# Optimization experiments

Hardware: AMD Instinct MI355X
Metric: run time of the kernel (lower is better)

Reference implementation:

```python
import jax, jax.numpy as jnp
import numpy as np

# Fuzzy system constants (from _init_fuzzy_system)
X1_C = jnp.arange(5.0)                 # x1 gauss centers 0,1,2,3,4 ; sigma 1
X2_C = jnp.arange(5.0) * 45.0          # x2 gauss centers 0,45,90,135,180 ; sigma 45
OUT_C = jnp.array([-0.3, 0.1, 0.5, 0.9, 1.3], dtype=jnp.float32)  # consequent centers ; sigma 0.3
Z = jnp.asarray(np.arange(-0.3, 1.31, 0.01), dtype=jnp.float32)   # 161-pt output universe

# Mamdani rules: list per consequent level of (x1_level, x2_level) OR-terms, levels XS..XL = 0..4
RULES = [
    [(2, 4), (3, 4), (3, 3), (4, 3), (4, 4)],            # -> coupling XS
    [(1, 4), (2, 3), (3, 2), (4, 1)],                    # -> S
    [(0, 4), (1, 3), (2, 2), (3, 1), (4, 0)],            # -> M
    [(0, 3), (1, 2), (2, 1), (3, 0)],                    # -> L
    [(0, 2), (0, 1), (0, 0), (1, 1), (1, 0), (2, 0)],    # -> XL
]


def gauss(x, c, s):
    return jnp.exp(-0.5 * ((x - c) / s) ** 2)


def setup_inputs() -> dict:
    key = jax.random.key(0)
    k1, k2, k3, k4 = jax.random.split(key, 4)
    N, E, D = 50000, 1000000, 8
    h = jax.random.normal(k1, (N, D), dtype=jnp.float32)
    src_idx = jax.random.randint(k2, (E,), 0, N, dtype=jnp.int32)
    dst_idx = jax.random.randint(k3, (E,), 0, N, dtype=jnp.int32)
    etypes = jax.random.randint(k4, (E,), 0, 3, dtype=jnp.int32)
    return {"h": h, "src_idx": src_idx, "dst_idx": dst_idx, "etypes": etypes}


def reference(h, src_idx, dst_idx, etypes):
    # edge vector: dst['h'] - src['h']
    v = h[dst_idx] - h[src_idx]                       # [E, D]
    # Ante_generator: x1 = |v| (distance, clipped to universe), x2 = angle(v, e1) in degrees
    n = jnp.sqrt(jnp.sum(v * v, axis=-1) + 1e-12)     # [E]
    x1 = jnp.clip(n, 0.0, 4.0)
    cosang = jnp.clip(v[:, 0] / n, -0.999999, 0.999999)
    x2 = jnp.degrees(jnp.arccos(cosang))              # [E] in [0, 180]
    # antecedent memberships
    mu1 = gauss(x1[:, None], X1_C[None, :], 1.0)      # [E, 5]
    mu2 = gauss(x2[:, None], X2_C[None, :], 45.0)     # [E, 5]
    zmf = gauss(Z[None, :], OUT_C[:, None], 0.3)      # [5, 161]
    # Mamdani: rule activation = max over OR-terms of min(mu1, mu2);
    # implication = min(act, consequent mf); aggregation = max over rules
    agg = jnp.zeros((x1.shape[0], Z.shape[0]), dtype=h.dtype)  # [E, 161]
    for r, pairs in enumerate(RULES):
        act = jnp.max(
            jnp.stack([jnp.minimum(mu1[:, i], mu2[:, j]) for i, j in pairs], axis=-1),
            axis=-1,
        )                                             # [E]
        agg = jnp.maximum(agg, jnp.minimum(act[:, None], zmf[r][None, :]))
    # centroid defuzzification
    coupling_degree = jnp.sum(agg * Z[None, :], axis=-1) / jnp.sum(agg, axis=-1)
    return coupling_degree
```

## Files before the change

### kernel.cpp

```cpp
#include <hip/hip_runtime.h>
#include <hip/hip_fp16.h>

typedef int   vi4 __attribute__((ext_vector_type(4)));
typedef float vf4 __attribute__((ext_vector_type(4)));

static constexpr double cexp_taylor(double x) {
    double s = 1.0, t = 1.0;
    for (int i = 1; i < 40; ++i) { t = t * x / (double)i; s += t; }
    return s;
}
static constexpr double cpow_int(double b, long e) {
    double r = 1.0, p = b;
    while (e > 0) { if (e & 1) r *= p; p *= p; e >>= 1; }
    return r;
}
struct ZmfTab { float v[5][161]; };
static constexpr ZmfTab make_zmf() {
    ZmfTab t{};
    const double c0 = cexp_taylor(-1.0 / 1800.0);
    for (int r = 0; r < 5; ++r)
        for (int k = 0; k < 161; ++k) {
            long d = (long)(k - 40 * r);
            t.v[r][k] = (float)cpow_int(c0, d * d);
        }
    return t;
}
static constexpr ZmfTab ZMF = make_zmf();
static constexpr float ZCUT = 1e-4f;

__device__ __forceinline__ float fuzzy_F(float x1, float u)
{
    float m1[5], m2[5];
#pragma unroll
    for (int i = 0; i < 5; ++i) {
        float d1 = x1 - (float)i;
        float d2 = u  - (float)i;
        m1[i] = __expf(-0.5f * d1 * d1);
        m2[i] = __expf(-0.5f * d2 * d2);
    }

    float a0 = fmaxf(fmaxf(fminf(m1[2], m2[4]), fminf(m1[3], m2[4])),
               fmaxf(fminf(m1[3], m2[3]),
               fmaxf(fminf(m1[4], m2[3]), fminf(m1[4], m2[4]))));
    float a1 = fmaxf(fmaxf(fminf(m1[1], m2[4]), fminf(m1[2], m2[3])),
               fmaxf(fminf(m1[3], m2[2]), fminf(m1[4], m2[1])));
    float a2 = fmaxf(fmaxf(fminf(m1[0], m2[4]), fminf(m1[1], m2[3])),
               fmaxf(fminf(m1[2], m2[2]),
               fmaxf(fminf(m1[3], m2[1]), fminf(m1[4], m2[0]))));
    float a3 = fmaxf(fmaxf(fminf(m1[0], m2[3]), fminf(m1[1], m2[2])),
               fmaxf(fminf(m1[2], m2[1]), fminf(m1[3], m2[0])));
    float a4 = fmaxf(fmaxf(fmaxf(fminf(m1[0], m2[2]), fminf(m1[0], m2[1])),
               fmaxf(fminf(m1[0], m2[0]), fminf(m1[1], m2[1]))),
               fmaxf(fminf(m1[1], m2[0]), fminf(m1[2], m2[0])));
    float a[5] = {a0, a1, a2, a3, a4};

    float s0 = 0.0f, s1 = 0.0f;
#pragma unroll
    for (int k = 0; k < 161; ++k) {
        float m = -1.0f;
        bool first = true;
#pragma unroll
        for (int r = 0; r < 5; ++r) {
            if (ZMF.v[r][k] >= ZCUT) {
                float tmin = fminf(a[r], ZMF.v[r][k]);
                m = first ? tmin : fmaxf(m, tmin);
                first = false;
            }
        }
        s0 += m;
        s1 = fmaf(m, (float)k, s1);
    }
    return fmaf(0.01f, s1 / s0, -0.3f);
}

#define PN 70
#define VN 71
#define TAB_U4 ((PN * PN) / 2)

struct H8 { __half2 p0, p1, p2, p3; };

__global__ __launch_bounds__(256) void build_pack_kernel(
    const float4* __restrict__ h4, __half* __restrict__ gtab,
    __half2* __restrict__ hp, int N, int nA)
{
    int b = blockIdx.x;
    if (b < nA) {
        int idx = b * 256 + threadIdx.x;
        if (idx >= VN * VN) return;
        int i = idx / VN;
        int j = idx - i * VN;
        const float hstep = 4.0f / (float)PN;
        __half f = __float2half_rn(fuzzy_F((float)i * hstep, (float)j * hstep));
        if (i < PN && j < PN) gtab[4 * (i * PN + j) + 0]           = f;
        if (i < PN && j > 0)  gtab[4 * (i * PN + j - 1) + 1]       = f;
        if (i > 0 && j < PN)  gtab[4 * ((i - 1) * PN + j) + 2]     = f;
        if (i > 0 && j > 0)   gtab[4 * ((i - 1) * PN + j - 1) + 3] = f;
    } else {
        int r = (b - nA) * 256 + threadIdx.x;
        if (r >= N) return;
        float4 a = h4[2 * r], c = h4[2 * r + 1];
        __half2* o = hp + 4 * r;
        o[0] = __floats2half2_rn(a.x, a.y);
        o[1] = __floats2half2_rn(a.z, a.w);
        o[2] = __floats2half2_rn(c.x, c.y);
        o[3] = __floats2half2_rn(c.z, c.w);
    }
}

__device__ __forceinline__ float edge_eval(
    const H8* __restrict__ hp, const uint2* __restrict__ stab,
    int si, int di)
{
    H8 s = hp[si];
    H8 d = hp[di];

    float2 d0 = __half22float2(__hsub2(d.p0, s.p0));
    float2 d1 = __half22float2(__hsub2(d.p1, s.p1));
    float2 d2 = __half22float2(__hsub2(d.p2, s.p2));
    float2 d3 = __half22float2(__hsub2(d.p3, s.p3));

    float ss = fmaf(d0.x, d0.x, fmaf(d0.y, d0.y, fmaf(d1.x, d1.x, fmaf(d1.y, d1.y,
               fmaf(d2.x, d2.x, fmaf(d2.y, d2.y, fmaf(d3.x, d3.x,
               fmaf(d3.y, d3.y, 1e-12f))))))));

    float rn = rsqrtf(ss);
    float n  = ss * rn;
    float x1 = fminf(n, 4.0f);

    float c = d0.x * rn;
    c = fminf(fmaxf(c, -0.999999f), 0.999999f);

    float ac = fabsf(c);
    float t  = sqrtf(1.0f - ac);
    float p  = fmaf(fmaf(fmaf(-0.0187293f, ac, 0.0742610f), ac, -0.2121144f),
                    ac, 1.5707288f);
    float r0 = t * p;
    float acosv = (c < 0.0f) ? (3.14159265358979f - r0) : r0;
    float u = acosv * 1.27323954473516f;

    const float sc = (float)PN * 0.25f;
    float t1 = x1 * sc;
    float t2 = u  * sc;
    int i1 = min((int)t1, PN - 1);
    int i2 = min((int)t2, PN - 1);
    float f1 = t1 - (float)i1;
    float f2 = t2 - (float)i2;

    uint2 pk = stab[i1 * PN + i2];
    float2 lo2 = __half22float2(__builtin_bit_cast(__half2, pk.x));
    float2 hi2 = __half22float2(__builtin_bit_cast(__half2, pk.y));
    float lo = fmaf(f2, lo2.y - lo2.x, lo2.x);
    float hi = fmaf(f2, hi2.y - hi2.x, hi2.x);
    return fmaf(f1, hi - lo, lo);
}

__global__ __launch_bounds__(512, 8) void fuzzy_coupling_kernel(
    const H8*    __restrict__ hp,
    const int*   __restrict__ src,
    const int*   __restrict__ dst,
    const uint4* __restrict__ gtab4,
    float*       __restrict__ out,
    int E)
{
    __shared__ uint4 stab4[TAB_U4];
    for (int k = threadIdx.x; k < TAB_U4; k += 512) stab4[k] = gtab4[k];
    __syncthreads();
    const uint2* stab = (const uint2*)stab4;

    int t = blockIdx.x * 512 + threadIdx.x;
    int e0 = 4 * t;
    if (e0 >= E) return;

    if (e0 + 3 < E) {
        vi4 sp = __builtin_nontemporal_load((const vi4*)src + t);
        vi4 dp = __builtin_nontemporal_load((const vi4*)dst + t);
        float r0 = edge_eval(hp, stab, sp.x, dp.x);
        float r1 = edge_eval(hp, stab, sp.y, dp.y);
        float r2 = edge_eval(hp, stab, sp.z, dp.z);
        float r3 = edge_eval(hp, stab, sp.w, dp.w);
        vf4 res; res.x = r0; res.y = r1; res.z = r2; res.w = r3;
        __builtin_nontemporal_store(res, (vf4*)out + t);
    } else {
        for (int e = e0; e < E; ++e)
            out[e] = edge_eval(hp, stab, src[e], dst[e]);
    }
}

extern "C" void kernel_launch(void* const* d_in, const int* in_sizes, int n_in,
                              void* d_out, int out_size, void* d_ws, size_t ws_size,
                              hipStream_t stream)
{
    const float* h   = (const float*)d_in[0];
    const int*   src = (const int*)d_in[1];
    const int*   dst = (const int*)d_in[2];
    float* out = (float*)d_out;

    __half*  gtab = (__half*)d_ws;
    __half2* hp   = (__half2*)((char*)d_ws + 65536);

    int N = in_sizes[0] / 8;
    int E = in_sizes[1];

    int nA = (VN * VN + 255) / 256;
    int nB = (N + 255) / 256;
    build_pack_kernel<<<nA + nB, 256, 0, stream>>>(
        (const float4*)h, gtab, hp, N, nA);

    int threads = (E + 3) / 4;
    int grid = (threads + 511) / 512;
    fuzzy_coupling_kernel<<<grid, 512, 0, stream>>>(
        (const H8*)hp, src, dst, (const uint4*)gtab, out, E);
}
```

Measured before the change: 79.03 us.

## Store fuzzy lookup table as plain fp32 grid and process two edges per thread

Replaces the packed fp16 quad-corner lookup table with a plain fp32 (VN x VN) grid. Each lookup now does four LDS reads instead of one 8-byte read, and the table holds only the grid values, so the build kernel writes each value once. It also halves the edges per thread from four to two, doubling the thread and block count. That gives more parallelism for the random gathers, but each block now repeats the shared-table load for fewer edges, and the LDS reads per edge go up.

```diff
diff --git a/kernel.cpp b/kernel.cpp
--- a/kernel.cpp
+++ b/kernel.cpp
@@ -1,8 +1,8 @@
 #include <hip/hip_runtime.h>
 #include <hip/hip_fp16.h>
 
-typedef int   vi4 __attribute__((ext_vector_type(4)));
-typedef float vf4 __attribute__((ext_vector_type(4)));
+typedef int   vi2 __attribute__((ext_vector_type(2)));
+typedef float vf2 __attribute__((ext_vector_type(2)));
 
 static constexpr double cexp_taylor(double x) {
     double s = 1.0, t = 1.0;
@@ -75,12 +75,13 @@
 
 #define PN 70
 #define VN 71
-#define TAB_U4 ((PN * PN) / 2)
+#define TAB_F  ((VN * VN + 3) & ~3)
+#define TAB_U4 (TAB_F / 4)
 
 struct H8 { __half2 p0, p1, p2, p3; };
 
 __global__ __launch_bounds__(256) void build_pack_kernel(
-    const float4* __restrict__ h4, __half* __restrict__ gtab,
+    const float4* __restrict__ h4, float* __restrict__ gtab,
     __half2* __restrict__ hp, int N, int nA)
 {
     int b = blockIdx.x;
@@ -90,11 +91,7 @@
         int i = idx / VN;
         int j = idx - i * VN;
         const float hstep = 4.0f / (float)PN;
-        __half f = __float2half_rn(fuzzy_F((float)i * hstep, (float)j * hstep));
-        if (i < PN && j < PN) gtab[4 * (i * PN + j) + 0]           = f;
-        if (i < PN && j > 0)  gtab[4 * (i * PN + j - 1) + 1]       = f;
-        if (i > 0 && j < PN)  gtab[4 * ((i - 1) * PN + j) + 2]     = f;
-        if (i > 0 && j > 0)   gtab[4 * ((i - 1) * PN + j - 1) + 3] = f;
+        gtab[idx] = fuzzy_F((float)i * hstep, (float)j * hstep);
     } else {
         int r = (b - nA) * 256 + threadIdx.x;
         if (r >= N) return;
@@ -108,7 +105,7 @@
 }
 
 __device__ __forceinline__ float edge_eval(
-    const H8* __restrict__ hp, const uint2* __restrict__ stab,
+    const H8* __restrict__ hp, const float* __restrict__ stab,
     int si, int di)
 {
     H8 s = hp[si];
@@ -146,11 +143,13 @@
     float f1 = t1 - (float)i1;
     float f2 = t2 - (float)i2;
 
-    uint2 pk = stab[i1 * PN + i2];
-    float2 lo2 = __half22float2(__builtin_bit_cast(__half2, pk.x));
-    float2 hi2 = __half22float2(__builtin_bit_cast(__half2, pk.y));
-    float lo = fmaf(f2, lo2.y - lo2.x, lo2.x);
-    float hi = fmaf(f2, hi2.y - hi2.x, hi2.x);
+    const float* ptab = stab + (i1 * VN + i2);
+    float v00 = ptab[0];
+    float v01 = ptab[1];
+    float v10 = ptab[VN];
+    float v11 = ptab[VN + 1];
+    float lo = fmaf(f2, v01 - v00, v00);
+    float hi = fmaf(f2, v11 - v10, v10);
     return fmaf(f1, hi - lo, lo);
 }
 
@@ -162,27 +161,24 @@
     float*       __restrict__ out,
     int E)
 {
-    __shared__ uint4 stab4[TAB_U4];
-    for (int k = threadIdx.x; k < TAB_U4; k += 512) stab4[k] = gtab4[k];
+    __shared__ float stab[TAB_F];
+    uint4* s4 = (uint4*)stab;
+    for (int k = threadIdx.x; k < TAB_U4; k += 512) s4[k] = gtab4[k];
     __syncthreads();
-    const uint2* stab = (const uint2*)stab4;
 
     int t = blockIdx.x * 512 + threadIdx.x;
-    int e0 = 4 * t;
+    int e0 = 2 * t;
     if (e0 >= E) return;
 
-    if (e0 + 3 < E) {
-        vi4 sp = __builtin_nontemporal_load((const vi4*)src + t);
-        vi4 dp = __builtin_nontemporal_load((const vi4*)dst + t);
+    if (e0 + 1 < E) {
+        vi2 sp = __builtin_nontemporal_load((const vi2*)src + t);
+        vi2 dp = __builtin_nontemporal_load((const vi2*)dst + t);
         float r0 = edge_eval(hp, stab, sp.x, dp.x);
         float r1 = edge_eval(hp, stab, sp.y, dp.y);
-        float r2 = edge_eval(hp, stab, sp.z, dp.z);
-        float r3 = edge_eval(hp, stab, sp.w, dp.w);
-        vf4 res; res.x = r0; res.y = r1; res.z = r2; res.w = r3;
-        __builtin_nontemporal_store(res, (vf4*)out + t);
+        vf2 res; res.x = r0; res.y = r1;
+        __builtin_nontemporal_store(res, (vf2*)out + t);
     } else {
-        for (int e = e0; e < E; ++e)
-            out[e] = edge_eval(hp, stab, src[e], dst[e]);
+        out[e0] = edge_eval(hp, stab, src[e0], dst[e0]);
     }
 }
 
@@ -195,7 +191,7 @@
     const int*   dst = (const int*)d_in[2];
     float* out = (float*)d_out;
 
-    __half*  gtab = (__half*)d_ws;
+    float*   gtab = (float*)d_ws;
     __half2* hp   = (__half2*)((char*)d_ws + 65536);
 
     int N = in_sizes[0] / 8;
@@ -206,7 +202,7 @@
     build_pack_kernel<<<nA + nB, 256, 0, stream>>>(
         (const float4*)h, gtab, hp, N, nA);
 
-    int threads = (E + 3) / 4;
+    int threads = (E + 1) / 2;
     int grid = (threads + 511) / 512;
     fuzzy_coupling_kernel<<<grid, 512, 0, stream>>>(
         (const H8*)hp, src, dst, (const uint4*)gtab, out, E);
```

New measurement: 80.86 us. 2.3% more time.
